# Performance work log

Hardware: AMD Instinct MI355X
Metric: run time of the kernel (lower is better)

The kernel has to match this reference:

```python
import jax, jax.numpy as jnp
import numpy as np

B, N, C, H = 4, 1024, 1024, 16
D = C // H  # head_dim = 64
SCALE = D ** -0.5


def setup_inputs() -> dict:
    key = jax.random.key(0)
    ks = jax.random.split(key, 7)
    std = 0.02
    return {
        "xq": jax.random.normal(ks[0], (B, N, C), dtype=jnp.float32),
        "xk": jax.random.normal(ks[1], (B, N, C), dtype=jnp.float32),
        "xv": jax.random.normal(ks[2], (B, N, C), dtype=jnp.float32),
        # torch nn.Linear weights are [out_features, in_features]
        "Wq": jax.random.normal(ks[3], (C, C), dtype=jnp.float32) * std,
        "Wkv": jax.random.normal(ks[4], (2 * C, C), dtype=jnp.float32) * std,
        "Wp": jax.random.normal(ks[5], (C, C), dtype=jnp.float32) * std,
        "bp": jax.random.normal(ks[6], (C,), dtype=jnp.float32) * std,
    }


def reference(xq, xk, xv, Wq, Wkv, Wp, bp):
    b, nq, c = xq.shape
    nk = xk.shape[1]
    # q projection -> [B, H, Nq, D]
    q = (xq @ Wq.T).reshape(b, nq, H, D).transpose(0, 2, 1, 3)
    # HPA: shared projection produces K and V from xk (xv unused)
    kv = xk @ Wkv.T  # [B, Nk, 2C]
    k, v = jnp.split(kv, 2, axis=-1)
    k = k.reshape(b, nk, H, D).transpose(0, 2, 1, 3)  # [B, H, Nk, D]
    v = v.reshape(b, nk, H, D).transpose(0, 2, 1, 3)  # [B, H, Nk, D]
    # pre-softmax scores (attn_save in original)
    attn = jnp.einsum("bhqd,bhkd->bhqk", q, k) * SCALE  # [B, H, Nq, Nk]
    p = jax.nn.softmax(attn, axis=-1)
    x = jnp.einsum("bhqk,bhkd->bhqd", p, v)  # [B, H, Nq, D]
    x = x.transpose(0, 2, 1, 3).reshape(b, nq, c)
    x = x @ Wp.T + bp
    # returns (x transposed to [Nq, B, C], mean-over-heads pre-softmax scores)
    return x.transpose(1, 0, 2), attn.sum(axis=1) / H
```

## Files before the change

kernel.cpp:

```cpp
#include <hip/hip_runtime.h>
#include <hip/hip_bf16.h>
#include <stdint.h>

typedef __attribute__((ext_vector_type(8))) short bf16x8;
typedef __attribute__((ext_vector_type(4))) short bf16x4;
typedef __attribute__((ext_vector_type(4))) float f32x4;

#define B_DIM 4
#define N_DIM 1024
#define C_DIM 1024
#define NT 16

#define QSCALE 0.18033688011112042f
#define OUT1_ALPHA 0.04332169878499658f

__device__ __forceinline__ ushort f2bf(float f) {
  union { float f; uint32_t u; } v; v.f = f;
  uint32_t r = (v.u + 0x7FFFu + ((v.u >> 16) & 1u)) >> 16;
  return (ushort)r;
}

__device__ __forceinline__ uint32_t cvtpk(float lo, float hi) {
  uint32_t r;
  asm("v_cvt_pk_bf16_f32 %0, %1, %2" : "=v"(r) : "v"(lo), "v"(hi));
  return r;
}

__device__ __forceinline__ void gload_lds16(const void* g, void* l) {
  __builtin_amdgcn_global_load_lds(
      (const __attribute__((address_space(1))) void*)g,
      (__attribute__((address_space(3))) void*)l, 16, 0, 0);
}

__device__ __forceinline__ f32x4 mfma16(bf16x8 a, bf16x8 b, f32x4 c) {
  return __builtin_amdgcn_mfma_f32_16x16x32_bf16(a, b, c, 0, 0, 0);
}

__device__ __forceinline__ void mfma16x16(bf16x4 a, bf16x4 b, f32x4& c) {
  asm("v_mfma_f32_16x16x16_bf16 %0, %1, %2, %0" : "+v"(c) : "v"(a), "v"(b));
}

template <int N>
__device__ __forceinline__ void waitcnt_vm() {
  asm volatile("s_waitcnt vmcnt(%0)" ::"i"(N) : "memory");
}

__global__ __launch_bounds__(256) void cvt_all(
    const float* __restrict__ xq, const float* __restrict__ xk,
    const float* __restrict__ Wq, const float* __restrict__ Wkv,
    const float* __restrict__ Wp, ushort* __restrict__ xq_b,
    ushort* __restrict__ xk_b, ushort* __restrict__ Wq_b,
    ushort* __restrict__ Wkv_b, ushort* __restrict__ Wp_b) {
  int bid = blockIdx.x;
  const float* s;
  ushort* d;
  int off;
  if (bid < 4096) { s = xq; d = xq_b; off = bid; }
  else if (bid < 8192) { s = xk; d = xk_b; off = bid - 4096; }
  else if (bid < 9216) { s = Wq; d = Wq_b; off = bid - 8192; }
  else if (bid < 11264) { s = Wkv; d = Wkv_b; off = bid - 9216; }
  else { s = Wp; d = Wp_b; off = bid - 11264; }
  int i = off * 1024 + threadIdx.x * 4;
  float4 v = *(const float4*)(s + i);
  ushort4 o;
  o.x = f2bf(v.x); o.y = f2bf(v.y); o.z = f2bf(v.z); o.w = f2bf(v.w);
  *(ushort4*)(d + i) = o;
}

template <int MODE>
__device__ __forceinline__ void gemm_nb_core(
    ushort* Ls, const ushort* A, const ushort* Bm, int lda, int ldb,
    float* Cf, ushort* Cb, int ldc, int crow0, int ccol0, float alpha,
    const float* bias) {
  const int l = threadIdx.x & 63;
  const int lg = l >> 4, lr = l & 15;
  const int cs = ((l & 3) ^ ((l >> 3) & 3)) * 8;
  const ushort* Ar = A + (size_t)(l >> 2) * lda + cs;
  const ushort* Br = Bm + (size_t)(l >> 2) * ldb + cs;
  ushort* LA = Ls;
  ushort* LB = Ls + 4096;
  const int cA = (lg ^ ((lr >> 1) & 3)) << 3;

#define NBSTAGE(t, bi)                                          \
  {                                                             \
    const int k0_ = (t) << 5;                                   \
    gload_lds16(Ar + k0_, LA + (bi) * 2048);                    \
    gload_lds16(Ar + (size_t)16 * lda + k0_, LA + (bi) * 2048 + 512);  \
    gload_lds16(Ar + (size_t)32 * lda + k0_, LA + (bi) * 2048 + 1024); \
    gload_lds16(Ar + (size_t)48 * lda + k0_, LA + (bi) * 2048 + 1536); \
    gload_lds16(Br + k0_, LB + (bi) * 2048);                    \
    gload_lds16(Br + (size_t)16 * ldb + k0_, LB + (bi) * 2048 + 512);  \
    gload_lds16(Br + (size_t)32 * ldb + k0_, LB + (bi) * 2048 + 1024); \
    gload_lds16(Br + (size_t)48 * ldb + k0_, LB + (bi) * 2048 + 1536); \
  }

  f32x4 acc[4][4] = {};
  NBSTAGE(0, 0);
  NBSTAGE(1, 1);
  for (int t = 0; t < 32; ++t) {
    if (t + 1 < 32) waitcnt_vm<8>(); else waitcnt_vm<0>();
    const int bo = (t & 1) * 2048;
    bf16x8 af[4], bf[4];
#pragma unroll
    for (int m = 0; m < 4; m++)
      af[m] = *(const bf16x8*)&LA[bo + (m * 16 + lr) * 32 + cA];
#pragma unroll
    for (int n = 0; n < 4; n++)
      bf[n] = *(const bf16x8*)&LB[bo + (n * 16 + lr) * 32 + cA];
    __builtin_amdgcn_s_setprio(1);
#pragma unroll
    for (int m = 0; m < 4; m++)
#pragma unroll
      for (int n = 0; n < 4; n++)
        acc[m][n] = mfma16(af[m], bf[n], acc[m][n]);
    __builtin_amdgcn_s_setprio(0);
    if (t + 2 < 32) NBSTAGE(t + 2, t & 1);
  }
#undef NBSTAGE

#pragma unroll
  for (int m = 0; m < 4; m++) {
    const int row = crow0 + m * 16 + lg * 4;
#pragma unroll
    for (int n = 0; n < 4; n++) {
      const int col = ccol0 + n * 16 + lr;
#pragma unroll
      for (int r = 0; r < 4; r++) {
        float v = acc[m][n][r];
        if (MODE == 0) {
          Cb[(size_t)(row + r) * ldc + col] = f2bf(v * alpha);
        } else {
          int gm = row + r;
          int bb = gm >> 10, nq = gm & 1023;
          Cf[((size_t)nq * B_DIM + bb) * C_DIM + col] = v + bias[col];
        }
      }
    }
  }
}

__global__ __launch_bounds__(64) void gemm_nb_dual(
    const ushort* __restrict__ xq_b, const ushort* __restrict__ xk_b,
    const ushort* __restrict__ Wq_b, const ushort* __restrict__ Wkv_b,
    ushort* __restrict__ Qp, ushort* __restrict__ KVp) {
  __shared__ ushort Ls[8192];
  int bid = blockIdx.x;
  if (bid < 1024) {
    int mt = bid >> 4, nt = bid & 15;
    gemm_nb_core<0>(Ls, xq_b + (size_t)mt * 64 * 1024,
                    Wq_b + (size_t)nt * 64 * 1024, 1024, 1024, nullptr, Qp,
                    1024, mt * 64, nt * 64, QSCALE, nullptr);
  } else {
    int b2 = bid - 1024;
    int mt = b2 >> 5, nt = b2 & 31;
    gemm_nb_core<0>(Ls, xk_b + (size_t)mt * 64 * 1024,
                    Wkv_b + (size_t)nt * 64 * 1024, 1024, 1024, nullptr, KVp,
                    2048, mt * 64, nt * 64, 1.f, nullptr);
  }
}

__global__ __launch_bounds__(64) void gemm_nb_proj(
    const ushort* __restrict__ Ob, const ushort* __restrict__ Wp_b,
    float* __restrict__ out0, const float* __restrict__ bias) {
  __shared__ ushort Ls[8192];
  int bid = blockIdx.x;
  int mt = bid >> 4, nt = bid & 15;
  gemm_nb_core<2>(Ls, Ob + (size_t)mt * 64 * 1024,
                  Wp_b + (size_t)nt * 64 * 1024, 1024, 1024, out0, nullptr,
                  1024, mt * 64, nt * 64, 1.f, bias);
}

template <int MODE, int BN>
__device__ __forceinline__ void gemm_core(
    ushort* As, ushort* Bs, const ushort* A, const ushort* Bm, float* Cf,
    ushort* Cb, int K, int lda, int ldb, int ldc, int m0, int n0, float alpha,
    const float* bias) {
  constexpr int MR = (BN == 128) ? 4 : 2;
  constexpr int WM = (BN == 128) ? 64 : 32;
  constexpr int ABUF = 4096, BBUF = BN * 32;
  constexpr int NLD = (BN == 128) ? 4 : 3;
  const int tid = threadIdx.x;
  const int l = tid & 63, wv = tid >> 6, lg = l >> 4, lr = l & 15;
  const int wr = (BN == 128) ? (wv >> 1) : wv;
  const int wc = (BN == 128) ? (wv & 1) : 0;
  const int r0 = tid >> 2;
  const int cs = ((tid & 3) ^ ((r0 >> 1) & 3)) * 8;
  const int wb = (tid & ~63) * 8;
  const int cA = ((lg ^ ((lr >> 1) & 3)) << 3);
  const ushort* Ar0 = A + (size_t)(m0 + r0) * lda + cs;
  const ushort* Ar1 = A + (size_t)(m0 + 64 + r0) * lda + cs;
  const ushort* Br0 = Bm + (size_t)(n0 + r0) * ldb + cs;
  const ushort* Br1 = Bm + (size_t)(n0 + 64 + r0) * ldb + cs;

#define STAGE(t, bi)                                                     \
  {                                                                      \
    const int k0_ = (t) << 5;                                            \
    gload_lds16(Ar0 + k0_, As + (bi) * ABUF + wb);                       \
    gload_lds16(Ar1 + k0_, As + (bi) * ABUF + 2048 + wb);                \
    gload_lds16(Br0 + k0_, Bs + (bi) * BBUF + wb);                       \
    if (BN == 128) gload_lds16(Br1 + k0_, Bs + (bi) * BBUF + 2048 + wb); \
  }

  const int nk = K >> 5;
  STAGE(0, 0);
  STAGE(1, 1);
  f32x4 acc[MR][4] = {};
  waitcnt_vm<NLD>();
  __builtin_amdgcn_sched_barrier(0);
  __builtin_amdgcn_s_barrier();
  __builtin_amdgcn_sched_barrier(0);
  int b0 = 0;
  for (int t = 0; t < nk; ++t) {
    const int b2 = (b0 + 2 >= 3) ? b0 - 1 : b0 + 2;
    if (t + 2 < nk) STAGE(t + 2, b2);
    const ushort* Ab = As + b0 * ABUF;
    const ushort* Bb = Bs + b0 * BBUF;
    bf16x8 af[MR], bfr[4];
#pragma unroll
    for (int m = 0; m < MR; m++)
      af[m] = *(const bf16x8*)&Ab[(wr * WM + m * 16 + lr) * 32 + cA];
#pragma unroll
    for (int n = 0; n < 4; n++)
      bfr[n] = *(const bf16x8*)&Bb[(wc * 64 + n * 16 + lr) * 32 + cA];
    __builtin_amdgcn_s_setprio(1);
#pragma unroll
    for (int m = 0; m < MR; m++)
#pragma unroll
      for (int n = 0; n < 4; n++)
        acc[m][n] = mfma16(af[m], bfr[n], acc[m][n]);
    __builtin_amdgcn_s_setprio(0);
    if (t + 1 < nk) {
      if (t + 2 < nk) waitcnt_vm<NLD>(); else waitcnt_vm<0>();
      __builtin_amdgcn_sched_barrier(0);
      __builtin_amdgcn_s_barrier();
      __builtin_amdgcn_sched_barrier(0);
    }
    b0 = (b0 + 1 >= 3) ? 0 : b0 + 1;
  }
#undef STAGE

#pragma unroll
  for (int m = 0; m < MR; m++) {
    const int row = m0 + wr * WM + m * 16 + lg * 4;
#pragma unroll
    for (int n = 0; n < 4; n++) {
      const int col = n0 + wc * 64 + n * 16 + lr;
#pragma unroll
      for (int r = 0; r < 4; r++) {
        float v = acc[m][n][r];
        if (MODE == 0) {
          Cb[(size_t)(row + r) * ldc + col] = f2bf(v * alpha);
        } else if (MODE == 1) {
          Cf[(size_t)(row + r) * ldc + col] = v * alpha;
        } else {
          int gm = row + r;
          int bb = gm >> 10, nq = gm & 1023;
          Cf[((size_t)nq * B_DIM + bb) * C_DIM + col] = v + bias[col];
        }
      }
    }
  }
}

__global__ __launch_bounds__(256) void flash_out1(
    const ushort* __restrict__ Qp, const ushort* __restrict__ KVp,
    ushort* __restrict__ O, float* __restrict__ out1) {
  __shared__ ushort sm[20480];
  int bid = blockIdx.x;

  if (bid >= 1024) {
    int b2 = bid - 1024;
    int z = b2 >> 7;
    gemm_core<1, 64>(sm, sm + 12288, Qp + (size_t)z * 1048576,
                     KVp + (size_t)z * 2097152, out1 + (size_t)z * 1048576,
                     nullptr, 1024, 1024, 2048, 1024, ((b2 >> 4) & 7) * 128,
                     (b2 & 15) * 64, OUT1_ALPHA, nullptr);
    return;
  }

  ushort* Ks0 = sm;
  ushort* Vs0 = sm + 8192;
  ushort* Qs = sm + 16384;

  const int tid = threadIdx.x;
  const int w = tid >> 6, l = tid & 63;
  const int lg = l >> 4, lr = l & 15;
  const int bh = bid >> 4;
  const int b = bh >> 4, h = bh & 15;
  const int q0 = (bid & 15) * 64;

  const ushort* Qg =
      Qp + (size_t)b * (N_DIM * C_DIM) + (size_t)q0 * C_DIM + h * 64;
  const ushort* Kg = KVp + (size_t)b * (N_DIM * 2 * C_DIM) + h * 64;
  const ushort* Vg = Kg + C_DIM;

  const int sr = tid >> 3;
  const int sc = (tid & 7) ^ (sr & 7);
  const int wb = (tid & ~63) * 8;
  const int vrow = (l & 31) >> 1;
  const int vdc = ((l >> 5) << 4) + (l & 1) * 8;

#define STAGE_K(kt2, buf)                                                   \
  {                                                                         \
    gload_lds16(Kg + (size_t)((kt2) + sr) * 2048 + sc * 8, (buf) + wb);     \
    gload_lds16(Kg + (size_t)((kt2) + 32 + sr) * 2048 + sc * 8,             \
                (buf) + 2048 + wb);                                         \
  }
#define STAGE_V(kt2, buf)                                                   \
  {                                                                         \
    gload_lds16(Vg + (size_t)((kt2) + w * 16 + vrow) * 2048 + vdc,          \
                (buf) + (w * 4 + 0) * 256);                                 \
    gload_lds16(Vg + (size_t)((kt2) + w * 16 + vrow) * 2048 + 32 + vdc,     \
                (buf) + (w * 4 + 2) * 256);                                 \
  }

  gload_lds16(Qg + (size_t)sr * C_DIM + sc * 8, Qs + wb);
  gload_lds16(Qg + (size_t)(32 + sr) * C_DIM + sc * 8, Qs + 2048 + wb);
  STAGE_K(0, Ks0);
  STAGE_V(0, Vs0);
  __syncthreads();
  const int qrow = w * 16 + lr;
  bf16x8 qa0 = *(const bf16x8*)&Qs[qrow * 64 + ((lg ^ (qrow & 7)) << 3)];
  bf16x8 qa1 = *(const bf16x8*)&Qs[qrow * 64 + (((lg + 4) ^ (qrow & 7)) << 3)];

  f32x4 oacc[4] = {};
  float lp = 0.f;
  const uint32_t vbase =
      (uint32_t)(uintptr_t)(__attribute__((address_space(3))) ushort*)Vs0 +
      (uint32_t)(l * 8);

  for (int t = 0; t < NT; ++t) {
    const int cur = t & 1;
    ushort* Kc = Ks0 + cur * 4096;
    if (t + 1 < NT) {
      const int kt2 = (t + 1) * 64;
      STAGE_K(kt2, Ks0 + (cur ^ 1) * 4096);
      STAGE_V(kt2, Vs0 + (cur ^ 1) * 4096);
    }

    f32x4 s[4];
    __builtin_amdgcn_s_setprio(1);
#pragma unroll
    for (int kf = 0; kf < 4; kf++) {
      const int krow = kf * 16 + lr;
      bf16x8 kb0 = *(const bf16x8*)&Kc[krow * 64 + ((lg ^ (krow & 7)) << 3)];
      bf16x8 kb1 =
          *(const bf16x8*)&Kc[krow * 64 + (((lg + 4) ^ (krow & 7)) << 3)];
      f32x4 zz = {};
      zz = mfma16(kb0, qa0, zz);
      zz = mfma16(kb1, qa1, zz);
      s[kf] = zz;
    }
    __builtin_amdgcn_s_setprio(0);

    bf16x4 pa[4];
#pragma unroll
    for (int kf = 0; kf < 4; kf++) {
      float p0 = exp2f(s[kf][0]), p1 = exp2f(s[kf][1]);
      float p2 = exp2f(s[kf][2]), p3 = exp2f(s[kf][3]);
      lp += (p0 + p1) + (p2 + p3);
      union { uint32_t u[2]; bf16x4 v; } pk;
      pk.u[0] = cvtpk(p0, p1);
      pk.u[1] = cvtpk(p2, p3);
      pa[kf] = pk.v;
    }

    const uint32_t trb = vbase + cur * 8192;
    __builtin_amdgcn_s_setprio(1);
#define PV_DF(df, O0, O1, O2, O3)                                          \
  {                                                                        \
    bf16x4 v0, v1, v2, v3;                                                 \
    asm volatile("ds_read_b64_tr_b16 %0, %1 offset:" #O0                   \
                 : "=v"(v0) : "v"(trb));                                   \
    asm volatile("ds_read_b64_tr_b16 %0, %1 offset:" #O1                   \
                 : "=v"(v1) : "v"(trb));                                   \
    asm volatile("ds_read_b64_tr_b16 %0, %1 offset:" #O2                   \
                 : "=v"(v2) : "v"(trb));                                   \
    asm volatile("ds_read_b64_tr_b16 %0, %1 offset:" #O3                   \
                 : "=v"(v3) : "v"(trb));                                   \
    asm volatile("s_waitcnt lgkmcnt(0)" ::: "memory");                     \
    __builtin_amdgcn_sched_barrier(0);                                     \
    mfma16x16(pa[0], v0, oacc[df]);                                        \
    mfma16x16(pa[1], v1, oacc[df]);                                        \
    mfma16x16(pa[2], v2, oacc[df]);                                        \
    mfma16x16(pa[3], v3, oacc[df]);                                        \
  }
    PV_DF(0, 0, 2048, 4096, 6144)
    PV_DF(1, 512, 2560, 4608, 6656)
    PV_DF(2, 1024, 3072, 5120, 7168)
    PV_DF(3, 1536, 3584, 5632, 7680)
#undef PV_DF
    __builtin_amdgcn_s_setprio(0);

    __syncthreads();
  }
#undef STAGE_K
#undef STAGE_V

  lp += __shfl_xor(lp, 16);
  lp += __shfl_xor(lp, 32);
  float linv[4];
#pragma unroll
  for (int r = 0; r < 4; r++) linv[r] = 1.0f / __shfl(lp, lg * 4 + r);

  ushort* Og = O + (size_t)b * (N_DIM * C_DIM) +
               (size_t)(q0 + w * 16 + lg * 4) * C_DIM + h * 64;
#pragma unroll
  for (int df = 0; df < 4; df++)
#pragma unroll
    for (int r = 0; r < 4; r++)
      Og[(size_t)r * C_DIM + df * 16 + lr] = f2bf(oacc[df][r] * linv[r]);
}

extern "C" void kernel_launch(void* const* d_in, const int* in_sizes, int n_in,
                              void* d_out, int out_size, void* d_ws,
                              size_t ws_size, hipStream_t stream) {
  const float* xq = (const float*)d_in[0];
  const float* xk = (const float*)d_in[1];
  const float* Wq = (const float*)d_in[3];
  const float* Wkv = (const float*)d_in[4];
  const float* Wp = (const float*)d_in[5];
  const float* bp = (const float*)d_in[6];

  ushort* ws = (ushort*)d_ws;
  ushort* xq_b = ws;
  ushort* xk_b = xq_b + 4194304;
  ushort* Wq_b = xk_b + 4194304;
  ushort* Wkv_b = Wq_b + 1048576;
  ushort* Wp_b = Wkv_b + 2097152;
  ushort* Qp = Wp_b + 1048576;
  ushort* KVp = Qp + 4194304;
  ushort* Ob = KVp + 8388608;

  float* out0 = (float*)d_out;
  float* out1 = out0 + 4194304;

  cvt_all<<<12288, 256, 0, stream>>>(xq, xk, Wq, Wkv, Wp, xq_b, xk_b, Wq_b,
                                     Wkv_b, Wp_b);
  gemm_nb_dual<<<3072, 64, 0, stream>>>(xq_b, xk_b, Wq_b, Wkv_b, Qp, KVp);
  flash_out1<<<1536, 256, 0, stream>>>(Qp, KVp, Ob, out1);
  gemm_nb_proj<<<1024, 64, 0, stream>>>(Ob, Wp_b, out0, bp);
}
```

Before: 228.2 us.

## Use 128x64 tiled 4-wave GEMM for output projection and remap dual-GEMM block order

Replaces the single-wave 64x64 output projection GEMM with a 256-thread kernel computing 128x64 tiles, using double-buffered direct-to-LDS loads. This is meant to raise operand reuse and reduce the block count. It also permutes block indices in the Q/KV projection kernel so consecutive block IDs are spread across the 8 groups (likely XCDs), which may improve cache locality. The new LDS layout has no swizzle, so it risks bank conflicts.

Result: no change. 226.7 us (-0.6%).

```diff
diff --git a/kernel.cpp b/kernel.cpp
--- a/kernel.cpp
+++ b/kernel.cpp
@@ -144,7 +144,7 @@
     const ushort* __restrict__ Wq_b, const ushort* __restrict__ Wkv_b,
     ushort* __restrict__ Qp, ushort* __restrict__ KVp) {
   __shared__ ushort Ls[8192];
-  int bid = blockIdx.x;
+  int bid = (blockIdx.x & 7) * 384 + (blockIdx.x >> 3);
   if (bid < 1024) {
     int mt = bid >> 4, nt = bid & 15;
     gemm_nb_core<0>(Ls, xq_b + (size_t)mt * 64 * 1024,
@@ -159,15 +159,91 @@
   }
 }
 
-__global__ __launch_bounds__(64) void gemm_nb_proj(
-    const ushort* __restrict__ Ob, const ushort* __restrict__ Wp_b,
-    float* __restrict__ out0, const float* __restrict__ bias) {
-  __shared__ ushort Ls[8192];
-  int bid = blockIdx.x;
-  int mt = bid >> 4, nt = bid & 15;
-  gemm_nb_core<2>(Ls, Ob + (size_t)mt * 64 * 1024,
-                  Wp_b + (size_t)nt * 64 * 1024, 1024, 1024, out0, nullptr,
-                  1024, mt * 64, nt * 64, 1.f, bias);
+template <int MODE, int BN>
+__device__ __forceinline__ void gemm2_core(
+    ushort* As, ushort* Bs, const ushort* A, const ushort* Bm, float* Cf,
+    ushort* Cb, int K, int lda, int ldb, int ldc, int m0, int n0, float alpha,
+    const float* bias) {
+  constexpr int MR = (BN == 128) ? 4 : 2;
+  constexpr int WM = (BN == 128) ? 64 : 32;
+  constexpr int BBUF = BN * 32;
+  const int tid = threadIdx.x;
+  const int l = tid & 63, wv = tid >> 6, lg = l >> 4, lr = l & 15;
+  const int wr = (BN == 128) ? (wv >> 1) : wv;
+  const int wc = (BN == 128) ? (wv & 1) : 0;
+  const int r0 = tid >> 2, c0 = (tid & 3) * 8;
+  const int wb = (tid & ~63) * 8;
+  const ushort* Arow0 = A + (size_t)(m0 + r0) * lda + c0;
+  const ushort* Arow1 = A + (size_t)(m0 + 64 + r0) * lda + c0;
+  const ushort* Brow0 = Bm + (size_t)(n0 + r0) * ldb + c0;
+  const ushort* Brow1 =
+      (BN == 128) ? (Bm + (size_t)(n0 + 64 + r0) * ldb + c0) : Brow0;
+
+  gload_lds16(Arow0, As + wb);
+  gload_lds16(Arow1, As + 2048 + wb);
+  gload_lds16(Brow0, Bs + wb);
+  if (BN == 128) gload_lds16(Brow1, Bs + 2048 + wb);
+  f32x4 acc[MR][4] = {};
+  __syncthreads();
+  const int nk = K >> 5;
+  for (int t = 0; t < nk; ++t) {
+    const int pA = (t & 1) ? 4096 : 0;
+    const int pB = (t & 1) ? BBUF : 0;
+    if (t + 1 < nk) {
+      const int nA = pA ^ 4096, nB = pB ^ BBUF;
+      const int k0 = (t + 1) << 5;
+      gload_lds16(Arow0 + k0, As + nA + wb);
+      gload_lds16(Arow1 + k0, As + nA + 2048 + wb);
+      gload_lds16(Brow0 + k0, Bs + nB + wb);
+      if (BN == 128) gload_lds16(Brow1 + k0, Bs + nB + 2048 + wb);
+    }
+    bf16x8 af[MR], bfr[4];
+#pragma unroll
+    for (int m = 0; m < MR; m++)
+      af[m] = *(const bf16x8*)&As[pA + (wr * WM + m * 16 + lr) * 32 + lg * 8];
+#pragma unroll
+    for (int n = 0; n < 4; n++)
+      bfr[n] = *(const bf16x8*)&Bs[pB + (wc * 64 + n * 16 + lr) * 32 + lg * 8];
+#pragma unroll
+    for (int m = 0; m < MR; m++)
+#pragma unroll
+      for (int n = 0; n < 4; n++)
+        acc[m][n] = mfma16(af[m], bfr[n], acc[m][n]);
+    __syncthreads();
+  }
+
+#pragma unroll
+  for (int m = 0; m < MR; m++) {
+    const int row = m0 + wr * WM + m * 16 + lg * 4;
+#pragma unroll
+    for (int n = 0; n < 4; n++) {
+      const int col = n0 + wc * 64 + n * 16 + lr;
+#pragma unroll
+      for (int r = 0; r < 4; r++) {
+        float v = acc[m][n][r];
+        if (MODE == 0) {
+          Cb[(size_t)(row + r) * ldc + col] = f2bf(v * alpha);
+        } else if (MODE == 1) {
+          Cf[(size_t)(row + r) * ldc + col] = v * alpha;
+        } else {
+          int gm = row + r;
+          int bb = gm >> 10, nq = gm & 1023;
+          Cf[((size_t)nq * B_DIM + bb) * C_DIM + col] = v + bias[col];
+        }
+      }
+    }
+  }
+}
+
+template <int MODE, int BN>
+__global__ __launch_bounds__(256) void gemm2_bt(
+    const ushort* __restrict__ A, const ushort* __restrict__ Bm,
+    float* __restrict__ Cf, ushort* __restrict__ Cb, int K, int lda, int ldb,
+    int ldc, float alpha, const float* __restrict__ bias) {
+  __shared__ ushort As[2 * 4096];
+  __shared__ ushort Bs[2 * BN * 32];
+  gemm2_core<MODE, BN>(As, Bs, A, Bm, Cf, Cb, K, lda, ldb, ldc,
+                       blockIdx.y * 128, blockIdx.x * BN, alpha, bias);
 }
 
 template <int MODE, int BN>
@@ -439,5 +515,6 @@
                                      Wkv_b, Wp_b);
   gemm_nb_dual<<<3072, 64, 0, stream>>>(xq_b, xk_b, Wq_b, Wkv_b, Qp, KVp);
   flash_out1<<<1536, 256, 0, stream>>>(Qp, KVp, Ob, out1);
-  gemm_nb_proj<<<1024, 64, 0, stream>>>(Ob, Wp_b, out0, bp);
-}
+  gemm2_bt<2, 64><<<dim3(16, 32, 1), 256, 0, stream>>>(
+      Ob, Wp_b, out0, nullptr, 1024, 1024, 1024, 1024, 1.f, bp);
+}
```

## Replace LDS-staged GEMM with direct register loads and XCD-aware block remap

Applied to the files above, without the earlier changes.

The projection GEMMs stop staging A/B tiles through LDS with async global-to-LDS loads and double buffering. Each lane now reads its MFMA fragments straight from global memory into registers in a fully unrolled K loop. Block indices are remapped so neighbouring tiles land on the same XCD for L2 reuse, and launch bounds request three waves per SIMD. This removes LDS traffic and waitcnt synchronisation, at the cost of uncoalesced 16-byte global reads, no explicit prefetch, and higher register pressure from the unrolled loop.

Result: slower. 275.9 us (+20.9%).

```diff
diff --git a/kernel.cpp b/kernel.cpp
--- a/kernel.cpp
+++ b/kernel.cpp
@@ -68,55 +68,33 @@
 }
 
 template <int MODE>
-__device__ __forceinline__ void gemm_nb_core(
-    ushort* Ls, const ushort* A, const ushort* Bm, int lda, int ldb,
-    float* Cf, ushort* Cb, int ldc, int crow0, int ccol0, float alpha,
+__device__ __forceinline__ void gemm_rd_core(
+    const ushort* A, const ushort* Bm, int lda, int ldb, float* Cf,
+    ushort* Cb, int ldc, int crow0, int ccol0, float alpha,
     const float* bias) {
   const int l = threadIdx.x & 63;
   const int lg = l >> 4, lr = l & 15;
-  const int cs = ((l & 3) ^ ((l >> 3) & 3)) * 8;
-  const ushort* Ar = A + (size_t)(l >> 2) * lda + cs;
-  const ushort* Br = Bm + (size_t)(l >> 2) * ldb + cs;
-  ushort* LA = Ls;
-  ushort* LB = Ls + 4096;
-  const int cA = (lg ^ ((lr >> 1) & 3)) << 3;
-
-#define NBSTAGE(t, bi)                                          \
-  {                                                             \
-    const int k0_ = (t) << 5;                                   \
-    gload_lds16(Ar + k0_, LA + (bi) * 2048);                    \
-    gload_lds16(Ar + (size_t)16 * lda + k0_, LA + (bi) * 2048 + 512);  \
-    gload_lds16(Ar + (size_t)32 * lda + k0_, LA + (bi) * 2048 + 1024); \
-    gload_lds16(Ar + (size_t)48 * lda + k0_, LA + (bi) * 2048 + 1536); \
-    gload_lds16(Br + k0_, LB + (bi) * 2048);                    \
-    gload_lds16(Br + (size_t)16 * ldb + k0_, LB + (bi) * 2048 + 512);  \
-    gload_lds16(Br + (size_t)32 * ldb + k0_, LB + (bi) * 2048 + 1024); \
-    gload_lds16(Br + (size_t)48 * ldb + k0_, LB + (bi) * 2048 + 1536); \
-  }
+  const ushort* Ap[4];
+  const ushort* Bp[4];
+#pragma unroll
+  for (int m = 0; m < 4; m++) Ap[m] = A + (size_t)(m * 16 + lr) * lda + lg * 8;
+#pragma unroll
+  for (int n = 0; n < 4; n++) Bp[n] = Bm + (size_t)(n * 16 + lr) * ldb + lg * 8;
 
   f32x4 acc[4][4] = {};
-  NBSTAGE(0, 0);
-  NBSTAGE(1, 1);
+#pragma unroll
   for (int t = 0; t < 32; ++t) {
-    if (t + 1 < 32) waitcnt_vm<8>(); else waitcnt_vm<0>();
-    const int bo = (t & 1) * 2048;
-    bf16x8 af[4], bf[4];
+    bf16x8 af[4], bfv[4];
+#pragma unroll
+    for (int m = 0; m < 4; m++) af[m] = *(const bf16x8*)(Ap[m] + t * 32);
+#pragma unroll
+    for (int n = 0; n < 4; n++) bfv[n] = *(const bf16x8*)(Bp[n] + t * 32);
 #pragma unroll
     for (int m = 0; m < 4; m++)
-      af[m] = *(const bf16x8*)&LA[bo + (m * 16 + lr) * 32 + cA];
-#pragma unroll
-    for (int n = 0; n < 4; n++)
-      bf[n] = *(const bf16x8*)&LB[bo + (n * 16 + lr) * 32 + cA];
-    __builtin_amdgcn_s_setprio(1);
-#pragma unroll
-    for (int m = 0; m < 4; m++)
 #pragma unroll
       for (int n = 0; n < 4; n++)
-        acc[m][n] = mfma16(af[m], bf[n], acc[m][n]);
-    __builtin_amdgcn_s_setprio(0);
-    if (t + 2 < 32) NBSTAGE(t + 2, t & 1);
-  }
-#undef NBSTAGE
+        acc[m][n] = mfma16(af[m], bfv[n], acc[m][n]);
+  }
 
 #pragma unroll
   for (int m = 0; m < 4; m++) {
@@ -139,35 +117,33 @@
   }
 }
 
-__global__ __launch_bounds__(64) void gemm_nb_dual(
+__global__ __launch_bounds__(64, 3) void gemm_rd_dual(
     const ushort* __restrict__ xq_b, const ushort* __restrict__ xk_b,
     const ushort* __restrict__ Wq_b, const ushort* __restrict__ Wkv_b,
     ushort* __restrict__ Qp, ushort* __restrict__ KVp) {
-  __shared__ ushort Ls[8192];
-  int bid = blockIdx.x;
+  int bid = (blockIdx.x & 7) * 384 + (blockIdx.x >> 3);
   if (bid < 1024) {
     int mt = bid >> 4, nt = bid & 15;
-    gemm_nb_core<0>(Ls, xq_b + (size_t)mt * 64 * 1024,
+    gemm_rd_core<0>(xq_b + (size_t)mt * 64 * 1024,
                     Wq_b + (size_t)nt * 64 * 1024, 1024, 1024, nullptr, Qp,
                     1024, mt * 64, nt * 64, QSCALE, nullptr);
   } else {
     int b2 = bid - 1024;
     int mt = b2 >> 5, nt = b2 & 31;
-    gemm_nb_core<0>(Ls, xk_b + (size_t)mt * 64 * 1024,
+    gemm_rd_core<0>(xk_b + (size_t)mt * 64 * 1024,
                     Wkv_b + (size_t)nt * 64 * 1024, 1024, 1024, nullptr, KVp,
                     2048, mt * 64, nt * 64, 1.f, nullptr);
   }
 }
 
-__global__ __launch_bounds__(64) void gemm_nb_proj(
+__global__ __launch_bounds__(64, 3) void gemm_rd_proj(
     const ushort* __restrict__ Ob, const ushort* __restrict__ Wp_b,
     float* __restrict__ out0, const float* __restrict__ bias) {
-  __shared__ ushort Ls[8192];
-  int bid = blockIdx.x;
+  int bid = (blockIdx.x & 7) * 128 + (blockIdx.x >> 3);
   int mt = bid >> 4, nt = bid & 15;
-  gemm_nb_core<2>(Ls, Ob + (size_t)mt * 64 * 1024,
-                  Wp_b + (size_t)nt * 64 * 1024, 1024, 1024, out0, nullptr,
-                  1024, mt * 64, nt * 64, 1.f, bias);
+  gemm_rd_core<2>(Ob + (size_t)mt * 64 * 1024, Wp_b + (size_t)nt * 64 * 1024,
+                  1024, 1024, out0, nullptr, 1024, mt * 64, nt * 64, 1.f,
+                  bias);
 }
 
 template <int MODE, int BN>
@@ -437,7 +413,7 @@
 
   cvt_all<<<12288, 256, 0, stream>>>(xq, xk, Wq, Wkv, Wp, xq_b, xk_b, Wq_b,
                                      Wkv_b, Wp_b);
-  gemm_nb_dual<<<3072, 64, 0, stream>>>(xq_b, xk_b, Wq_b, Wkv_b, Qp, KVp);
+  gemm_rd_dual<<<3072, 64, 0, stream>>>(xq_b, xk_b, Wq_b, Wkv_b, Qp, KVp);
   flash_out1<<<1536, 256, 0, stream>>>(Qp, KVp, Ob, out1);
-  gemm_nb_proj<<<1024, 64, 0, stream>>>(Ob, Wp_b, out0, bp);
-}
+  gemm_rd_proj<<<1024, 64, 0, stream>>>(Ob, Wp_b, out0, bp);
+}
```
